# Performance work log

Measured on AMD Instinct MI355X. Metric: run time of the kernel, lower is better.

## Reference

```python
import jax, jax.numpy as jnp
import numpy as np

B, L, H, NH = 8, 256, 128, 4
D = H // NH
NEG = jnp.float32(-(2.0 ** 32) + 1.0)


def setup_inputs() -> dict:
    key = jax.random.key(0)
    ks = jax.random.split(key, 12)
    f = lambda k, s, sc=1.0: jax.random.normal(k, s, dtype=jnp.float32) * sc
    inp = {
        "queries": f(ks[0], (B, L, H)),
        "keys": f(ks[1], (B, L, H)),
        "time_matrix_K": f(ks[2], (B, L, L, H), 0.05),
        "time_matrix_V": f(ks[3], (B, L, L, H), 0.05),
        "abs_pos_K": f(ks[4], (B, L, H), 0.1),
        "abs_pos_V": f(ks[5], (B, L, H), 0.1),
        "Wq": f(ks[6], (H, H), 1.0 / np.sqrt(H)),
        "bq": jnp.zeros((H,), jnp.float32),
        "Wk": f(ks[7], (H, H), 1.0 / np.sqrt(H)),
        "bk": jnp.zeros((H,), jnp.float32),
        "Wv": f(ks[8], (H, H), 1.0 / np.sqrt(H)),
        "bv": jnp.zeros((H,), jnp.float32),
        # True = padded query row (masked out)
        "time_mask": jax.random.uniform(ks[9], (B, L)) < 0.1,
        # causal mask: True above the diagonal = not attendable
        "attn_mask": jnp.triu(jnp.ones((L, L), dtype=bool), k=1),
    }
    return inp


def reference(queries, keys, time_matrix_K, time_matrix_V, abs_pos_K, abs_pos_V,
              Wq, bq, Wk, bk, Wv, bv, time_mask, attn_mask):
    # Linear projections (torch Linear: x @ W.T + b)
    Q = queries @ Wq.T + bq
    K = keys @ Wk.T + bk
    V = keys @ Wv.T + bv
    # head split: channels [i*D:(i+1)*D] -> head i  (equivalent to torch split/cat)
    Qh = Q.reshape(B, L, NH, D)
    Kh = K.reshape(B, L, NH, D)
    Vh = V.reshape(B, L, NH, D)
    pKh = abs_pos_K.reshape(B, L, NH, D)
    pVh = abs_pos_V.reshape(B, L, NH, D)
    tKh = time_matrix_K.reshape(B, L, L, NH, D)
    tVh = time_matrix_V.reshape(B, L, L, NH, D)
    # scores: QK^T + Q*absposK^T + per-row time-interval bias  -> [B,NH,L,L]
    aw = jnp.einsum('blhd,bmhd->bhlm', Qh, Kh)
    aw += jnp.einsum('blhd,bmhd->bhlm', Qh, pKh)
    aw += jnp.einsum('blmhd,blhd->bhlm', tKh, Qh)
    aw = aw * jnp.float32(1.0 / np.sqrt(D))
    mask = time_mask[:, None, :, None] | attn_mask[None, None, :, :]
    aw = jnp.where(mask, NEG, aw)
    A = jax.nn.softmax(aw, axis=-1)  # dropout omitted (eval mode)
    # outputs: A@V + A@absposV + per-row A @ time_matrix_V  -> [B,L,NH,D]
    out = jnp.einsum('bhlm,bmhd->blhd', A, Vh)
    out += jnp.einsum('bhlm,bmhd->blhd', A, pVh)
    out += jnp.einsum('bhlm,blmhd->blhd', A, tVh)
    return out.reshape(B, L, H)
```

## Files before the change

### kernel.cpp

```cpp
#include <hip/hip_runtime.h>
#include <math.h>

#define Bdim 8
#define Lq   256
#define Hd   128

static constexpr float kNEG = -4294967295.0f;
static constexpr float kScale = 0.17677669529663687f;
static constexpr float kUni = 0.00390625f;

typedef float f32x4 __attribute__((ext_vector_type(4)));

__device__ __forceinline__ f32x4 nt4(const float* p) {
    return __builtin_nontemporal_load((const f32x4*)p);
}

__global__ __launch_bounds__(256) void prep_kernel(
    const float* __restrict__ Wq, const float* __restrict__ Wk,
    const float* __restrict__ Wv, const unsigned char* __restrict__ raw,
    float* __restrict__ Wt, int* __restrict__ outmask)
{
    const int blk = blockIdx.x;
    if (blk < 12) {
        __shared__ float tile[64][65];
        const int mi = blk >> 2;
        const float* W = (mi == 0) ? Wq : (mi == 1) ? Wk : Wv;
        float* WT = Wt + mi * (Hd * Hd);
        const int ti = blk & 3;
        const int r0 = (ti >> 1) * 64, c0 = (ti & 1) * 64;
        #pragma unroll
        for (int k = 0; k < 16; ++k) {
            const int e = threadIdx.x + k * 256;
            const int r = e >> 6, c = e & 63;
            tile[r][c] = W[(r0 + r) * Hd + (c0 + c)];
        }
        __syncthreads();
        #pragma unroll
        for (int k = 0; k < 16; ++k) {
            const int e = threadIdx.x + k * 256;
            const int r = e >> 6, c = e & 63;
            WT[(c0 + r) * Hd + (r0 + c)] = tile[c][r];
        }
    } else {
        __shared__ int cnt;
        if (threadIdx.x == 0) cnt = 0;
        __syncthreads();
        const int n = Bdim * Lq;
        for (int i = threadIdx.x; i < n; i += 256)
            if ((i & 3) && raw[i]) atomicAdd(&cnt, 1);
        __syncthreads();
        const bool is_u8 = (cnt > 0);
        const int* raw32 = (const int*)raw;
        for (int i = threadIdx.x; i < n; i += 256) {
            const int v = is_u8 ? (int)raw[i] : raw32[i];
            outmask[i] = (v != 0) ? 1 : 0;
        }
    }
}

__global__ __launch_bounds__(512) void proj_kernel(
    const float* __restrict__ queries, const float* __restrict__ keys,
    const float* __restrict__ absK, const float* __restrict__ absV,
    const float* __restrict__ Wt,
    const float* __restrict__ bq, const float* __restrict__ bk,
    const float* __restrict__ bv,
    float* __restrict__ Qb, float* __restrict__ Kb, float* __restrict__ Vb)
{
    constexpr int R = 8;
    __shared__ float xq[R][Hd];
    __shared__ float xk[R][Hd];
    const int row0 = blockIdx.x * R;
    const int tid = threadIdx.x;
    #pragma unroll
    for (int k = 0; k < 2; ++k) {
        const int e = tid + k * 512;
        const int r = e >> 7, c = e & 127;
        xq[r][c] = queries[(row0 + r) * Hd + c];
        xk[r][c] = keys[(row0 + r) * Hd + c];
    }
    __syncthreads();

    const int o = tid & 127, rh = tid >> 7;
    const int r0 = rh * 2, r1 = rh * 2 + 1;
    const float* __restrict__ Wtq = Wt;
    const float* __restrict__ Wtk = Wt + Hd * Hd;
    const float* __restrict__ Wtv = Wt + 2 * Hd * Hd;

    float qa0 = bq[o], qa1 = qa0;
    float ka0 = bk[o] + absK[(row0 + r0) * Hd + o];
    float ka1 = bk[o] + absK[(row0 + r1) * Hd + o];
    float va0 = bv[o] + absV[(row0 + r0) * Hd + o];
    float va1 = bv[o] + absV[(row0 + r1) * Hd + o];

    #pragma unroll 4
    for (int i = 0; i < Hd; ++i) {
        const float wq = Wtq[i * Hd + o];
        const float wk = Wtk[i * Hd + o];
        const float wv = Wtv[i * Hd + o];
        const float x0 = xq[r0][i], x1 = xq[r1][i];
        const float y0 = xk[r0][i], y1 = xk[r1][i];
        qa0 += x0 * wq; qa1 += x1 * wq;
        ka0 += y0 * wk; ka1 += y1 * wk;
        va0 += y0 * wv; va1 += y1 * wv;
    }
    Qb[(row0 + r0) * Hd + o] = qa0;  Qb[(row0 + r1) * Hd + o] = qa1;
    Kb[(row0 + r0) * Hd + o] = ka0;  Kb[(row0 + r1) * Hd + o] = ka1;
    Vb[(row0 + r0) * Hd + o] = va0;  Vb[(row0 + r1) * Hd + o] = va1;
}

__global__ __launch_bounds__(256) void attn_kernel(
    const float* __restrict__ Qb, const float* __restrict__ Kb,
    const float* __restrict__ Vb,
    const float* __restrict__ tK, const float* __restrict__ tV,
    const int* __restrict__ tmask, float* __restrict__ out)
{
    const int bid = blockIdx.x;
    const int b  = bid & 7;
    const int hp = (bid >> 3) & 1;
    const int j  = bid >> 4;

    const int tid = threadIdx.x;
    const int w = tid >> 6;
    const int h = hp * 2 + (w & 1);
    const int p = j * 2 + (w >> 1);
    const int l0 = p;
    const int l1 = 255 - p;
    const int m_off = (tid >> 2) & 15;
    const int cg = tid & 3;
    const int ch = h * 32 + cg * 8;

    const float* q0b = Qb + ((size_t)b * Lq + l0) * Hd + ch;
    const float* q1b = Qb + ((size_t)b * Lq + l1) * Hd + ch;
    f32x4 q00 = *(const f32x4*)q0b, q01 = *(const f32x4*)(q0b + 4);
    f32x4 q10 = *(const f32x4*)q1b, q11 = *(const f32x4*)(q1b + 4);
    q00 *= kScale; q01 *= kScale; q10 *= kScale; q11 *= kScale;

    const bool mk0 = (tmask[b * Lq + l0] != 0);
    const bool mk1 = (tmask[b * Lq + l1] != 0);
    const int ntc0 = (l0 >> 4) + 1, ntc1 = (l1 >> 4) + 1;
    const int n10 = mk0 ? 0 : ntc0, n11 = mk1 ? 0 : ntc1;
    const int NT1 = (n10 > n11) ? n10 : n11;
    const int n20 = mk0 ? 16 : ntc0, n21 = mk1 ? 16 : ntc1;
    const int NT2 = (n20 > n21) ? n20 : n21;

    const float* kpt = Kb + (size_t)b * Lq * Hd + m_off * Hd + ch;
    const float* vpt = Vb + (size_t)b * Lq * Hd + m_off * Hd + ch;
    const float* t0p = tK + (((size_t)b * Lq + l0) * Lq + m_off) * Hd + ch;
    const float* t1p = tK + (((size_t)b * Lq + l1) * Lq + m_off) * Hd + ch;
    const float* u0p = tV + (((size_t)b * Lq + l0) * Lq + m_off) * Hd + ch;
    const float* u1p = tV + (((size_t)b * Lq + l1) * Lq + m_off) * Hd + ch;

    float s0[16], s1[16];
    #pragma unroll
    for (int t = 0; t < 16; ++t) { s0[t] = kNEG; s1[t] = kNEG; }

    #pragma unroll
    for (int t = 0; t < 16; ++t) {
        if (t < NT1) {
            const f32x4 ka = *(const f32x4*)(kpt + t * 2048);
            const f32x4 kb = *(const f32x4*)(kpt + t * 2048 + 4);
            const int m = t * 16 + m_off;
            if (t < n10) {
                const f32x4 sa = ka + nt4(t0p + t * 2048);
                const f32x4 sb = kb + nt4(t0p + t * 2048 + 4);
                float pp = q00.x*sa.x + q00.y*sa.y + q00.z*sa.z + q00.w*sa.w
                         + q01.x*sb.x + q01.y*sb.y + q01.z*sb.z + q01.w*sb.w;
                pp += __shfl_xor(pp, 1);
                pp += __shfl_xor(pp, 2);
                s0[t] = (m <= l0) ? pp : kNEG;
            }
            if (t < n11) {
                const f32x4 sa = ka + nt4(t1p + t * 2048);
                const f32x4 sb = kb + nt4(t1p + t * 2048 + 4);
                float pp = q10.x*sa.x + q10.y*sa.y + q10.z*sa.z + q10.w*sa.w
                         + q11.x*sb.x + q11.y*sb.y + q11.z*sb.z + q11.w*sb.w;
                pp += __shfl_xor(pp, 1);
                pp += __shfl_xor(pp, 2);
                s1[t] = (m <= l1) ? pp : kNEG;
            }
        }
    }

    if (!mk0) {
        float mx = s0[0];
        #pragma unroll
        for (int t = 1; t < 16; ++t) mx = fmaxf(mx, s0[t]);
        #pragma unroll
        for (int d = 4; d < 64; d <<= 1) mx = fmaxf(mx, __shfl_xor(mx, d));
        float sum = 0.f;
        #pragma unroll
        for (int t = 0; t < 16; ++t) { s0[t] = expf(s0[t] - mx); sum += s0[t]; }
        #pragma unroll
        for (int d = 4; d < 64; d <<= 1) sum += __shfl_xor(sum, d);
        const float inv = 1.0f / sum;
        #pragma unroll
        for (int t = 0; t < 16; ++t) s0[t] *= inv;
    } else {
        #pragma unroll
        for (int t = 0; t < 16; ++t) s0[t] = kUni;
    }
    if (!mk1) {
        float mx = s1[0];
        #pragma unroll
        for (int t = 1; t < 16; ++t) mx = fmaxf(mx, s1[t]);
        #pragma unroll
        for (int d = 4; d < 64; d <<= 1) mx = fmaxf(mx, __shfl_xor(mx, d));
        float sum = 0.f;
        #pragma unroll
        for (int t = 0; t < 16; ++t) { s1[t] = expf(s1[t] - mx); sum += s1[t]; }
        #pragma unroll
        for (int d = 4; d < 64; d <<= 1) sum += __shfl_xor(sum, d);
        const float inv = 1.0f / sum;
        #pragma unroll
        for (int t = 0; t < 16; ++t) s1[t] *= inv;
    } else {
        #pragma unroll
        for (int t = 0; t < 16; ++t) s1[t] = kUni;
    }

    f32x4 a00 = {0,0,0,0}, a01 = {0,0,0,0};
    f32x4 a10 = {0,0,0,0}, a11 = {0,0,0,0};
    #pragma unroll
    for (int t = 0; t < 16; ++t) {
        if (t < NT2) {
            const f32x4 va = *(const f32x4*)(vpt + t * 2048);
            const f32x4 vb = *(const f32x4*)(vpt + t * 2048 + 4);
            if (t < n20) {
                const f32x4 ta = nt4(u0p + t * 2048);
                const f32x4 tb = nt4(u0p + t * 2048 + 4);
                const float aw = s0[t];
                a00 += aw * (va + ta);
                a01 += aw * (vb + tb);
            }
            if (t < n21) {
                const f32x4 ta = nt4(u1p + t * 2048);
                const f32x4 tb = nt4(u1p + t * 2048 + 4);
                const float aw = s1[t];
                a10 += aw * (va + ta);
                a11 += aw * (vb + tb);
            }
        }
    }
    #pragma unroll
    for (int d = 4; d < 64; d <<= 1) {
        a00.x += __shfl_xor(a00.x, d); a00.y += __shfl_xor(a00.y, d);
        a00.z += __shfl_xor(a00.z, d); a00.w += __shfl_xor(a00.w, d);
        a01.x += __shfl_xor(a01.x, d); a01.y += __shfl_xor(a01.y, d);
        a01.z += __shfl_xor(a01.z, d); a01.w += __shfl_xor(a01.w, d);
        a10.x += __shfl_xor(a10.x, d); a10.y += __shfl_xor(a10.y, d);
        a10.z += __shfl_xor(a10.z, d); a10.w += __shfl_xor(a10.w, d);
        a11.x += __shfl_xor(a11.x, d); a11.y += __shfl_xor(a11.y, d);
        a11.z += __shfl_xor(a11.z, d); a11.w += __shfl_xor(a11.w, d);
    }
    if (m_off == 0) {
        float* o0 = out + ((size_t)b * Lq + l0) * Hd + ch;
        *(f32x4*)o0 = a00; *(f32x4*)(o0 + 4) = a01;
        float* o1 = out + ((size_t)b * Lq + l1) * Hd + ch;
        *(f32x4*)o1 = a10; *(f32x4*)(o1 + 4) = a11;
    }
}

extern "C" void kernel_launch(void* const* d_in, const int* in_sizes, int n_in,
                              void* d_out, int out_size, void* d_ws, size_t ws_size,
                              hipStream_t stream) {
    const float* queries = (const float*)d_in[0];
    const float* keys    = (const float*)d_in[1];
    const float* tK      = (const float*)d_in[2];
    const float* tV      = (const float*)d_in[3];
    const float* absK    = (const float*)d_in[4];
    const float* absV    = (const float*)d_in[5];
    const float* Wq      = (const float*)d_in[6];
    const float* bq      = (const float*)d_in[7];
    const float* Wk      = (const float*)d_in[8];
    const float* bk      = (const float*)d_in[9];
    const float* Wv      = (const float*)d_in[10];
    const float* bv      = (const float*)d_in[11];
    const unsigned char* tmask_raw = (const unsigned char*)d_in[12];

    float* outp = (float*)d_out;

    const int rows = Bdim * Lq;
    float* Qb = (float*)d_ws;
    float* Kb = Qb + (size_t)rows * Hd;
    float* Vb = Kb + (size_t)rows * Hd;
    int* tmask = (int*)(Vb + (size_t)rows * Hd);
    float* Wt = (float*)(tmask + rows);

    prep_kernel<<<13, 256, 0, stream>>>(Wq, Wk, Wv, tmask_raw, Wt, tmask);
    proj_kernel<<<rows / 8, 512, 0, stream>>>(queries, keys, absK, absV, Wt,
                                              bq, bk, bv, Qb, Kb, Vb);
    attn_kernel<<<1024, 256, 0, stream>>>(Qb, Kb, Vb, tK, tV, tmask, outp);
}
```

Baseline: 92.38 us.

## Stage per-head K and V tiles in LDS and drop nontemporal loads

Restructures the attention kernel into 512-thread blocks where eight waves share one (batch, head) and cooperatively load that head's K, then V, slice into shared memory. This replaces repeated per-wave global K/V loads with LDS reads. It also switches the streamed time-matrix loads from nontemporal to ordinary loads. The extra barriers and the changed caching hint for the large tK/tV streams may offset the gain.

```diff
diff --git a/kernel.cpp b/kernel.cpp
--- a/kernel.cpp
+++ b/kernel.cpp
@@ -10,10 +10,6 @@
 static constexpr float kUni = 0.00390625f;
 
 typedef float f32x4 __attribute__((ext_vector_type(4)));
-
-__device__ __forceinline__ f32x4 nt4(const float* p) {
-    return __builtin_nontemporal_load((const f32x4*)p);
-}
 
 __global__ __launch_bounds__(256) void prep_kernel(
     const float* __restrict__ Wq, const float* __restrict__ Wk,
@@ -108,32 +104,41 @@
     Vb[(row0 + r0) * Hd + o] = va0;  Vb[(row0 + r1) * Hd + o] = va1;
 }
 
-__global__ __launch_bounds__(256) void attn_kernel(
+__global__ __launch_bounds__(512, 4) void attn_kernel(
     const float* __restrict__ Qb, const float* __restrict__ Kb,
     const float* __restrict__ Vb,
     const float* __restrict__ tK, const float* __restrict__ tV,
     const int* __restrict__ tmask, float* __restrict__ out)
 {
     const int bid = blockIdx.x;
-    const int b  = bid & 7;
-    const int hp = (bid >> 3) & 1;
-    const int j  = bid >> 4;
-
+    const int b = bid & 7;
+    const int h = (bid >> 3) & 3;
+    const int g = bid >> 5;
     const int tid = threadIdx.x;
     const int w = tid >> 6;
-    const int h = hp * 2 + (w & 1);
-    const int p = j * 2 + (w >> 1);
-    const int l0 = p;
-    const int l1 = 255 - p;
-    const int m_off = (tid >> 2) & 15;
-    const int cg = tid & 3;
+    const int lane = tid & 63;
+    const int p = g * 8 + w;
+    const int l0 = p, l1 = 255 - p;
+    const int m_off = (lane >> 2) & 15;
+    const int cg = lane & 3;
     const int ch = h * 32 + cg * 8;
+
+    __shared__ float S[256 * 36];
+
+    {
+        const int r = tid >> 1, half = tid & 1;
+        const float* src = Kb + ((size_t)(b * Lq + r)) * Hd + h * 32 + half * 16;
+        float* dst = &S[r * 36 + half * 16];
+        #pragma unroll
+        for (int qq = 0; qq < 4; ++qq)
+            *(f32x4*)(dst + qq * 4) = *(const f32x4*)(src + qq * 4);
+    }
+    __syncthreads();
 
     const float* q0b = Qb + ((size_t)b * Lq + l0) * Hd + ch;
     const float* q1b = Qb + ((size_t)b * Lq + l1) * Hd + ch;
-    f32x4 q00 = *(const f32x4*)q0b, q01 = *(const f32x4*)(q0b + 4);
-    f32x4 q10 = *(const f32x4*)q1b, q11 = *(const f32x4*)(q1b + 4);
-    q00 *= kScale; q01 *= kScale; q10 *= kScale; q11 *= kScale;
+    f32x4 q00 = *(const f32x4*)q0b * kScale, q01 = *(const f32x4*)(q0b + 4) * kScale;
+    f32x4 q10 = *(const f32x4*)q1b * kScale, q11 = *(const f32x4*)(q1b + 4) * kScale;
 
     const bool mk0 = (tmask[b * Lq + l0] != 0);
     const bool mk1 = (tmask[b * Lq + l1] != 0);
@@ -143,13 +148,13 @@
     const int n20 = mk0 ? 16 : ntc0, n21 = mk1 ? 16 : ntc1;
     const int NT2 = (n20 > n21) ? n20 : n21;
 
-    const float* kpt = Kb + (size_t)b * Lq * Hd + m_off * Hd + ch;
-    const float* vpt = Vb + (size_t)b * Lq * Hd + m_off * Hd + ch;
     const float* t0p = tK + (((size_t)b * Lq + l0) * Lq + m_off) * Hd + ch;
     const float* t1p = tK + (((size_t)b * Lq + l1) * Lq + m_off) * Hd + ch;
     const float* u0p = tV + (((size_t)b * Lq + l0) * Lq + m_off) * Hd + ch;
     const float* u1p = tV + (((size_t)b * Lq + l1) * Lq + m_off) * Hd + ch;
 
+    const float* kls = &S[m_off * 36 + cg * 8];
+
     float s0[16], s1[16];
     #pragma unroll
     for (int t = 0; t < 16; ++t) { s0[t] = kNEG; s1[t] = kNEG; }
@@ -157,12 +162,12 @@
     #pragma unroll
     for (int t = 0; t < 16; ++t) {
         if (t < NT1) {
-            const f32x4 ka = *(const f32x4*)(kpt + t * 2048);
-            const f32x4 kb = *(const f32x4*)(kpt + t * 2048 + 4);
+            const f32x4 ka = *(const f32x4*)(kls + t * 576);
+            const f32x4 kb = *(const f32x4*)(kls + t * 576 + 4);
             const int m = t * 16 + m_off;
             if (t < n10) {
-                const f32x4 sa = ka + nt4(t0p + t * 2048);
-                const f32x4 sb = kb + nt4(t0p + t * 2048 + 4);
+                const f32x4 sa = ka + *(const f32x4*)(t0p + t * 2048);
+                const f32x4 sb = kb + *(const f32x4*)(t0p + t * 2048 + 4);
                 float pp = q00.x*sa.x + q00.y*sa.y + q00.z*sa.z + q00.w*sa.w
                          + q01.x*sb.x + q01.y*sb.y + q01.z*sb.z + q01.w*sb.w;
                 pp += __shfl_xor(pp, 1);
@@ -170,8 +175,8 @@
                 s0[t] = (m <= l0) ? pp : kNEG;
             }
             if (t < n11) {
-                const f32x4 sa = ka + nt4(t1p + t * 2048);
-                const f32x4 sb = kb + nt4(t1p + t * 2048 + 4);
+                const f32x4 sa = ka + *(const f32x4*)(t1p + t * 2048);
+                const f32x4 sb = kb + *(const f32x4*)(t1p + t * 2048 + 4);
                 float pp = q10.x*sa.x + q10.y*sa.y + q10.z*sa.z + q10.w*sa.w
                          + q11.x*sb.x + q11.y*sb.y + q11.z*sb.z + q11.w*sb.w;
                 pp += __shfl_xor(pp, 1);
@@ -218,23 +223,35 @@
         for (int t = 0; t < 16; ++t) s1[t] = kUni;
     }
 
+    __syncthreads();
+
+    {
+        const int r = tid >> 1, half = tid & 1;
+        const float* src = Vb + ((size_t)(b * Lq + r)) * Hd + h * 32 + half * 16;
+        float* dst = &S[r * 36 + half * 16];
+        #pragma unroll
+        for (int qq = 0; qq < 4; ++qq)
+            *(f32x4*)(dst + qq * 4) = *(const f32x4*)(src + qq * 4);
+    }
+    __syncthreads();
+
     f32x4 a00 = {0,0,0,0}, a01 = {0,0,0,0};
     f32x4 a10 = {0,0,0,0}, a11 = {0,0,0,0};
     #pragma unroll
     for (int t = 0; t < 16; ++t) {
         if (t < NT2) {
-            const f32x4 va = *(const f32x4*)(vpt + t * 2048);
-            const f32x4 vb = *(const f32x4*)(vpt + t * 2048 + 4);
+            const f32x4 va = *(const f32x4*)(kls + t * 576);
+            const f32x4 vb = *(const f32x4*)(kls + t * 576 + 4);
             if (t < n20) {
-                const f32x4 ta = nt4(u0p + t * 2048);
-                const f32x4 tb = nt4(u0p + t * 2048 + 4);
+                const f32x4 ta = *(const f32x4*)(u0p + t * 2048);
+                const f32x4 tb = *(const f32x4*)(u0p + t * 2048 + 4);
                 const float aw = s0[t];
                 a00 += aw * (va + ta);
                 a01 += aw * (vb + tb);
             }
             if (t < n21) {
-                const f32x4 ta = nt4(u1p + t * 2048);
-                const f32x4 tb = nt4(u1p + t * 2048 + 4);
+                const f32x4 ta = *(const f32x4*)(u1p + t * 2048);
+                const f32x4 tb = *(const f32x4*)(u1p + t * 2048 + 4);
                 const float aw = s1[t];
                 a10 += aw * (va + ta);
                 a11 += aw * (vb + tb);
@@ -289,5 +306,5 @@
     prep_kernel<<<13, 256, 0, stream>>>(Wq, Wk, Wv, tmask_raw, Wt, tmask);
     proj_kernel<<<rows / 8, 512, 0, stream>>>(queries, keys, absK, absV, Wt,
                                               bq, bk, bv, Qb, Kb, Vb);
-    attn_kernel<<<1024, 256, 0, stream>>>(Qb, Kb, Vb, tK, tV, tmask, outp);
+    attn_kernel<<<512, 512, 0, stream>>>(Qb, Kb, Vb, tK, tV, tmask, outp);
 }
```

After: 81.07 us. 12.2% less time.
